# Optimization experiments

Measured on AMD Instinct MI355X. Metric: run time of the kernel, lower is better.

The kernel has to match this reference:

```python
import jax, jax.numpy as jnp
import numpy as np

V = 32000   # vocab / input_size
H = 1024    # hidden_size (== embedding dim)
L = 2       # num_layers
B = 64      # batch
T = 256     # seq_len


def setup_inputs() -> dict:
    key = jax.random.key(0)
    ks = jax.random.split(key, 8)
    s = float(1.0 / np.sqrt(H))  # pytorch default uniform bound for LSTM/Linear
    return {
        "inputs": jax.random.randint(ks[0], (B, T), 0, V),
        "embed_table": jax.random.normal(ks[1], (V, H), jnp.float32),
        "W_ih": jax.random.uniform(ks[2], (L, 4 * H, H), jnp.float32, -s, s),
        "W_hh": jax.random.uniform(ks[3], (L, 4 * H, H), jnp.float32, -s, s),
        "b_ih": jax.random.uniform(ks[4], (L, 4 * H), jnp.float32, -s, s),
        "b_hh": jax.random.uniform(ks[5], (L, 4 * H), jnp.float32, -s, s),
        "W_proj": jax.random.uniform(ks[6], (V, H), jnp.float32, -s, s),
        "b_proj": jnp.zeros((V,), jnp.float32),  # module fills bias with 0
    }


def _lstm_layer(x, Wih, Whh, bih, bhh):
    # x: [B, T, H]. Precompute input contribution for all steps (one big GEMM).
    xg = jnp.einsum("bth,gh->btg", x, Wih) + bih + bhh  # [B, T, 4H]
    h0 = jnp.zeros((x.shape[0], Whh.shape[1]), x.dtype)
    c0 = h0

    def step(carry, xt):
        h, c = carry
        gates = xt + h @ Whh.T  # [B, 4H]
        i, f, g, o = jnp.split(gates, 4, axis=-1)  # pytorch gate order i,f,g,o
        i = jax.nn.sigmoid(i)
        f = jax.nn.sigmoid(f)
        g = jnp.tanh(g)
        o = jax.nn.sigmoid(o)
        c = f * c + i * g
        h = o * jnp.tanh(c)
        return (h, c), h

    (hT, cT), ys = jax.lax.scan(step, (h0, c0), jnp.swapaxes(xg, 0, 1))
    return jnp.swapaxes(ys, 0, 1), hT, cT  # [B,T,H], [B,H], [B,H]


def reference(inputs, embed_table, W_ih, W_hh, b_ih, b_hh, W_proj, b_proj):
    x = embed_table[inputs]  # [B, T, H]
    h_n, c_n = [], []
    for l in range(L):  # small fixed layer loop
        x, hT, cT = _lstm_layer(x, W_ih[l], W_hh[l], b_ih[l], b_hh[l])
        h_n.append(hT)
        c_n.append(cT)
    last_output = x[:, -1]                      # squeeze(output[:, -1]) with B>1 -> [B, H]
    logits = last_output @ W_proj.T + b_proj    # [B, V]
    return last_output, logits, jnp.stack(h_n), jnp.stack(c_n)
```

## Files before the change

kernel.cpp:

```cpp
#include <hip/hip_runtime.h>
#include <hip/hip_bf16.h>
#include <stdint.h>
#include <stddef.h>

typedef __hip_bfloat16 bf16;
typedef __attribute__((ext_vector_type(8))) short bfrag;
typedef __attribute__((ext_vector_type(4))) float ffrag;

#define HDIM 1024
#define BATCH 64
#define TSTEPS 256
#define GDIM 4096
#define VOCAB 32000

#define HSLOT 16384ull

__device__ __forceinline__ float b2f(bf16 x) { return __bfloat162float(x); }
__device__ __forceinline__ bf16 f2b(float x) { return __float2bfloat16(x); }
__device__ __forceinline__ short f2bs(float x) {
  bf16 b = __float2bfloat16(x);
  return *reinterpret_cast<short*>(&b);
}
__device__ __forceinline__ float bs2f(unsigned short u) {
  union { unsigned int i; float f; } v;
  v.i = ((unsigned int)u) << 16;
  return v.f;
}
__device__ __forceinline__ ffrag mfma16(bfrag a, bfrag b, ffrag c) {
  return __builtin_amdgcn_mfma_f32_16x16x32_bf16(a, b, c, 0, 0, 0);
}
__device__ __forceinline__ float sigm(float x) { return 1.0f / (1.0f + __expf(-x)); }
__device__ __forceinline__ float tanhfast(float x) {
  float e = __expf(2.0f * x);
  return 1.0f - 2.0f / (e + 1.0f);
}

__device__ __forceinline__ void store_u16_agent(unsigned short* p, unsigned short v) {
  __hip_atomic_store(p, v, __ATOMIC_RELAXED, __HIP_MEMORY_SCOPE_AGENT);
}
__device__ __forceinline__ unsigned long long load_u64_agent(const unsigned long long* p) {
  return __hip_atomic_load(p, __ATOMIC_RELAXED, __HIP_MEMORY_SCOPE_AGENT);
}
__device__ __forceinline__ void store_u32_agent(unsigned* p, unsigned v) {
  __hip_atomic_store(p, v, __ATOMIC_RELAXED, __HIP_MEMORY_SCOPE_AGENT);
}

__global__ void convert_bf16_kernel(const float* __restrict__ src, bf16* __restrict__ dst, int n4) {
  int i = blockIdx.x * 256 + threadIdx.x;
  if (i >= n4) return;
  float4 v = reinterpret_cast<const float4*>(src)[i];
  ushort4 o;
  o.x = (unsigned short)f2bs(v.x);
  o.y = (unsigned short)f2bs(v.y);
  o.z = (unsigned short)f2bs(v.z);
  o.w = (unsigned short)f2bs(v.w);
  reinterpret_cast<ushort4*>(dst)[i] = o;
}

__global__ void embed_kernel(const int* __restrict__ ids, const float* __restrict__ table,
                             bf16* __restrict__ x, int n4) {
  int i = blockIdx.x * 256 + threadIdx.x;
  if (i >= n4) return;
  int row = i >> 8;
  int c4 = i & 255;
  int tok = ids[row];
  float4 v = reinterpret_cast<const float4*>(table)[(size_t)tok * 256 + c4];
  ushort4 o;
  o.x = (unsigned short)f2bs(v.x);
  o.y = (unsigned short)f2bs(v.y);
  o.z = (unsigned short)f2bs(v.z);
  o.w = (unsigned short)f2bs(v.w);
  reinterpret_cast<ushort4*>(x)[i] = o;
}

#define BMX 128
#define BNX 128
#define BKX 64

template<int LYR>
__launch_bounds__(256, 2)
__global__ void gemm_xg_kernel(const bf16* __restrict__ A,
                               const bf16* __restrict__ W,
                               const float* __restrict__ bih,
                               const float* __restrict__ bhh,
                               bf16* __restrict__ xg) {
  __shared__ bf16 As[BMX][BKX + 8];
  __shared__ bf16 Bs[BNX][BKX + 8];
  const int n0 = blockIdx.x * BNX;
  const int m0 = blockIdx.y * BMX;
  const int tid = threadIdx.x;
  const int w = tid >> 6, l = tid & 63;
  const int wm = (w >> 1) * 64, wn = (w & 1) * 64;
  const int lr = l & 15, lk = (l >> 4) * 8;

  ffrag acc[4][4];
#pragma unroll
  for (int i = 0; i < 4; ++i)
#pragma unroll
    for (int j = 0; j < 4; ++j) acc[i][j] = ffrag{0.f, 0.f, 0.f, 0.f};

  const int sr = tid >> 1, sh = (tid & 1) * 32;
  for (int kb = 0; kb < HDIM; kb += BKX) {
    __syncthreads();
    {
      if (LYR == 0) {
        const uint4* ga = reinterpret_cast<const uint4*>(&A[(size_t)(m0 + sr) * HDIM + kb + sh]);
        uint4* la = reinterpret_cast<uint4*>(&As[sr][sh]);
        la[0] = ga[0]; la[1] = ga[1]; la[2] = ga[2]; la[3] = ga[3];
      } else {
        const unsigned long long* hb = (const unsigned long long*)A;
        const int m = m0 + sr;
        const size_t tb = (size_t)(255 - (m >> 6)) * HSLOT + (m & 63);
        const int kg0 = (kb + sh) >> 3;
#pragma unroll
        for (int ii = 0; ii < 4; ++ii) {
          unsigned long long lo = hb[tb + (size_t)(kg0 + ii) * 64];
          unsigned long long hi = hb[tb + 8192 + (size_t)(kg0 + ii) * 64];
          *(unsigned long long*)&As[sr][sh + ii * 8]     = lo;
          *(unsigned long long*)&As[sr][sh + ii * 8 + 4] = hi;
        }
      }
      const uint4* gb = reinterpret_cast<const uint4*>(&W[(size_t)(n0 + sr) * HDIM + kb + sh]);
      uint4* lb = reinterpret_cast<uint4*>(&Bs[sr][sh]);
      lb[0] = gb[0]; lb[1] = gb[1]; lb[2] = gb[2]; lb[3] = gb[3];
    }
    __syncthreads();
#pragma unroll
    for (int ks = 0; ks < 2; ++ks) {
      const int ko = ks * 32 + lk;
      bfrag af[4], bfv[4];
#pragma unroll
      for (int i = 0; i < 4; ++i)
        af[i] = *reinterpret_cast<const bfrag*>(&As[wm + i * 16 + lr][ko]);
#pragma unroll
      for (int j = 0; j < 4; ++j)
        bfv[j] = *reinterpret_cast<const bfrag*>(&Bs[wn + j * 16 + lr][ko]);
#pragma unroll
      for (int i = 0; i < 4; ++i)
#pragma unroll
        for (int j = 0; j < 4; ++j)
          acc[i][j] = mfma16(af[i], bfv[j], acc[i][j]);
    }
  }
  const int rg = (l >> 4) * 4;
#pragma unroll
  for (int j = 0; j < 4; ++j) {
    const int n = n0 + wn + j * 16 + lr;
    const float bias = bih[n] + bhh[n];
    const int q = n >> 10, g = (n & 1023) >> 3, jj = n & 7;
    bf16* base = xg + (size_t)(q * 128 + g) * 16384 * 8 + jj;
#pragma unroll
    for (int i = 0; i < 4; ++i) {
#pragma unroll
      for (int r = 0; r < 4; ++r) {
        const int m = m0 + wm + i * 16 + rg + r;
        base[(size_t)m * 8] = f2b(acc[i][j][r] + bias);
      }
    }
  }
}

__launch_bounds__(128, 1)
__global__ void lstm_seq_kernel(const bf16* __restrict__ xg,
                                const bf16* __restrict__ Whh,
                                bf16* hist,
                                float* __restrict__ out_h,
                                float* __restrict__ out_c,
                                float* __restrict__ out_last,
                                unsigned* __restrict__ flags,
                                int xbs, int xts) {
  __shared__ float gxp[2][16][33];
  const int wgid = blockIdx.x;
  const int bg = wgid & 3, cg = wgid >> 2;
  const int tid = threadIdx.x;
  const int w = tid >> 6, l = tid & 63;
  const int lr = l & 15, lkg = l >> 4;
  const int kh = w, kbase = kh * 512;

  bfrag breg0[16], breg1[16];
  {
    const int q = lr >> 2, ja = lr & 3;
    const size_t g0 = ((size_t)q * HDIM + cg * 8 + ja) * HDIM + kbase + lkg * 8;
    const size_t g1 = ((size_t)q * HDIM + cg * 8 + 4 + ja) * HDIM + kbase + lkg * 8;
#pragma unroll
    for (int ks = 0; ks < 16; ++ks) {
      breg0[ks] = *reinterpret_cast<const bfrag*>(&Whh[g0 + ks * 32]);
      breg1[ks] = *reinterpret_cast<const bfrag*>(&Whh[g1 + ks * 32]);
    }
  }

  const int eb = tid & 15;
  const int ejj = tid >> 4;
  const int b_glob = bg * 16 + eb;
  const int j_glob = cg * 8 + ejj;
  const int set = ejj >> 2, jn = ejj & 3;
  float c = 0.0f;

  unsigned long long* hb = (unsigned long long*)hist;
  const size_t hbase = (size_t)(kh * 64 + lkg) * 64 + bg * 16 + lr;

  const bf16* xq0 = xg + (size_t)(0 * 128 + cg) * 16384 * 8 + ejj;
  const bf16* xq1 = xg + (size_t)(1 * 128 + cg) * 16384 * 8 + ejj;
  const bf16* xq2 = xg + (size_t)(2 * 128 + cg) * 16384 * 8 + ejj;
  const bf16* xq3 = xg + (size_t)(3 * 128 + cg) * 16384 * 8 + ejj;
  unsigned short xv0, xv1, xv2, xv3;
  {
    const size_t xidx = (size_t)b_glob * xbs;
    xv0 = *(const unsigned short*)&xq0[xidx * 8];
    xv1 = *(const unsigned short*)&xq1[xidx * 8];
    xv2 = *(const unsigned short*)&xq2[xidx * 8];
    xv3 = *(const unsigned short*)&xq3[xidx * 8];
  }

  const unsigned long long* fv = (const unsigned long long*)flags + (size_t)bg * 128;

#pragma unroll 1
  for (int t = 0; t < TSTEPS; ++t) {
    if (t > 0) {
      const unsigned tt = (unsigned)t;
      for (;;) {
        unsigned long long fa = load_u64_agent(&fv[l]);
        unsigned long long fb = load_u64_agent(&fv[64 + l]);
        int ok = ((unsigned)fa >= tt) && ((unsigned)(fa >> 32) >= tt) &&
                 ((unsigned)fb >= tt) && ((unsigned)(fb >> 32) >= tt);
        if (__all(ok)) break;
        __builtin_amdgcn_s_sleep(1);
      }
    }
    __builtin_amdgcn_sched_barrier(0);
    asm volatile("" ::: "memory");

    const unsigned long long* hin = hb + (size_t)(TSTEPS - t) * HSLOT;
    ffrag a0 = ffrag{0.f, 0.f, 0.f, 0.f};
    ffrag a1 = ffrag{0.f, 0.f, 0.f, 0.f};
#pragma unroll
    for (int ks = 0; ks < 16; ++ks) {
      union { unsigned long long u[2]; bfrag f; } au;
      au.u[0] = hin[hbase + ks * 256];
      au.u[1] = hin[8192 + hbase + ks * 256];
      a0 = mfma16(au.f, breg0[ks], a0);
      a1 = mfma16(au.f, breg1[ks], a1);
    }
#pragma unroll
    for (int r = 0; r < 4; ++r) {
      gxp[kh][lkg * 4 + r][lr]      = a0[r];
      gxp[kh][lkg * 4 + r][16 + lr] = a1[r];
    }
    __syncthreads();

    const float gi = gxp[0][eb][set * 16 + jn]      + gxp[1][eb][set * 16 + jn]      + bs2f(xv0);
    const float gf = gxp[0][eb][set * 16 + 4 + jn]  + gxp[1][eb][set * 16 + 4 + jn]  + bs2f(xv1);
    const float gg = gxp[0][eb][set * 16 + 8 + jn]  + gxp[1][eb][set * 16 + 8 + jn]  + bs2f(xv2);
    const float go = gxp[0][eb][set * 16 + 12 + jn] + gxp[1][eb][set * 16 + 12 + jn] + bs2f(xv3);
    const float iv = sigm(gi), fvv = sigm(gf), gv = tanhfast(gg), ov = sigm(go);
    c = fvv * c + iv * gv;
    const float h = ov * tanhfast(c);
    const unsigned short hbits = (unsigned short)f2bs(h);

    unsigned long long* hout = hb + (size_t)(255 - t) * HSLOT;
    unsigned short* hp = (unsigned short*)(hout + (size_t)set * 8192 + cg * 64 + b_glob) + jn;
    store_u16_agent(hp, hbits);

    if (t < TSTEPS - 1) {
      __builtin_amdgcn_s_waitcnt(0);
      if (l == 0) store_u32_agent(&flags[bg * 256 + cg * 2 + w], (unsigned)(t + 1));
      const size_t xidx = (size_t)b_glob * xbs + (size_t)(t + 1) * xts;
      xv0 = *(const unsigned short*)&xq0[xidx * 8];
      xv1 = *(const unsigned short*)&xq1[xidx * 8];
      xv2 = *(const unsigned short*)&xq2[xidx * 8];
      xv3 = *(const unsigned short*)&xq3[xidx * 8];
    } else {
      out_h[(size_t)b_glob * HDIM + j_glob] = h;
      out_c[(size_t)b_glob * HDIM + j_glob] = c;
      if (out_last) out_last[(size_t)b_glob * HDIM + j_glob] = h;
    }
  }
}

__launch_bounds__(256, 2)
__global__ void logits_kernel(const bf16* __restrict__ hfin,
                              const float* __restrict__ Wp,
                              const float* __restrict__ bp,
                              float* __restrict__ out) {
  const int tid = threadIdx.x;
  const int w = tid >> 6, l = tid & 63;
  const int lr = l & 15, lkg = l >> 4, lk = lkg * 8;
  const int col = blockIdx.x * 64 + w * 16 + lr;
  const float* wrow = &Wp[(size_t)col * HDIM];
  const unsigned long long* hb = (const unsigned long long*)hfin;
  ffrag acc[4];
#pragma unroll
  for (int i = 0; i < 4; ++i) acc[i] = ffrag{0.f, 0.f, 0.f, 0.f};
#pragma unroll 2
  for (int ks = 0; ks < 32; ++ks) {
    const int k = ks * 32 + lk;
    float4 wa = *reinterpret_cast<const float4*>(&wrow[k]);
    float4 wb = *reinterpret_cast<const float4*>(&wrow[k + 4]);
    bfrag bv;
    bv[0] = f2bs(wa.x); bv[1] = f2bs(wa.y); bv[2] = f2bs(wa.z); bv[3] = f2bs(wa.w);
    bv[4] = f2bs(wb.x); bv[5] = f2bs(wb.y); bv[6] = f2bs(wb.z); bv[7] = f2bs(wb.w);
    const size_t kg = (size_t)(ks * 4 + lkg);
#pragma unroll
    for (int i = 0; i < 4; ++i) {
      union { unsigned long long u[2]; bfrag f; } av;
      av.u[0] = hb[kg * 64 + i * 16 + lr];
      av.u[1] = hb[8192 + kg * 64 + i * 16 + lr];
      acc[i] = mfma16(av.f, bv, acc[i]);
    }
  }
  const float bias = bp[col];
#pragma unroll
  for (int i = 0; i < 4; ++i) {
#pragma unroll
    for (int r = 0; r < 4; ++r) {
      const int b = i * 16 + (l >> 4) * 4 + r;
      out[(size_t)b * VOCAB + col] = acc[i][r] + bias;
    }
  }
}

extern "C" void kernel_launch(void* const* d_in, const int* in_sizes, int n_in,
                              void* d_out, int out_size, void* d_ws, size_t ws_size,
                              hipStream_t stream) {
  const int*   ids   = (const int*)d_in[0];
  const float* table = (const float*)d_in[1];
  const float* Wih   = (const float*)d_in[2];
  const float* Whh   = (const float*)d_in[3];
  const float* bih   = (const float*)d_in[4];
  const float* bhh   = (const float*)d_in[5];
  const float* Wp    = (const float*)d_in[6];
  const float* bp    = (const float*)d_in[7];
  float* out = (float*)d_out;

  char* ws = (char*)d_ws;
  const size_t HISTB = 257ull * 131072ull;
  const size_t OFF_XG  = 0;
  const size_t OFF_HA  = OFF_XG + (size_t)512 * 16384 * 8 * 2;
  const size_t OFF_HB  = OFF_HA + HISTB;
  const size_t OFF_WIH = OFF_HB + HISTB;
  const size_t OFF_WHH = OFF_WIH + (size_t)2 * GDIM * HDIM * 2;
  const size_t OFF_SYNC= OFF_WHH + (size_t)2 * GDIM * HDIM * 2;

  bf16* xg    = (bf16*)(ws + OFF_XG);
  bf16* xb    = (bf16*)(ws + OFF_HA);
  bf16* histA = (bf16*)(ws + OFF_HA);
  bf16* histB = (bf16*)(ws + OFF_HB);
  bf16* wihb  = (bf16*)(ws + OFF_WIH);
  bf16* whhb  = (bf16*)(ws + OFF_WHH);
  unsigned* sync = (unsigned*)(ws + OFF_SYNC);

  (void)hipMemsetAsync(sync, 0, 16384, stream);
  (void)hipMemsetAsync(ws + OFF_HA + 33554432ull, 0, 131072, stream);
  (void)hipMemsetAsync(ws + OFF_HB + 33554432ull, 0, 131072, stream);

  const int nconv4 = 2 * GDIM * HDIM / 4;
  convert_bf16_kernel<<<nconv4 / 256, 256, 0, stream>>>(Wih, wihb, nconv4);
  convert_bf16_kernel<<<nconv4 / 256, 256, 0, stream>>>(Whh, whhb, nconv4);
  const int nemb4 = BATCH * TSTEPS * HDIM / 4;
  embed_kernel<<<nemb4 / 256, 256, 0, stream>>>(ids, table, xb, nemb4);

  float* out_last   = out;
  float* out_logits = out + 65536;
  float* out_hn     = out + 2113536;
  float* out_cn     = out + 2244608;

  gemm_xg_kernel<0><<<dim3(GDIM / BNX, (BATCH * TSTEPS) / BMX), 256, 0, stream>>>(
      xb, wihb, bih, bhh, xg);
  lstm_seq_kernel<<<512, 128, 0, stream>>>(
      xg, whhb, histA, out_hn, out_cn, nullptr, sync, 256, 1);

  gemm_xg_kernel<1><<<dim3(GDIM / BNX, (BATCH * TSTEPS) / BMX), 256, 0, stream>>>(
      histA, wihb + (size_t)GDIM * HDIM, bih + GDIM, bhh + GDIM, xg);
  lstm_seq_kernel<<<512, 128, 0, stream>>>(
      xg, whhb + (size_t)GDIM * HDIM, histB,
      out_hn + (size_t)BATCH * HDIM, out_cn + (size_t)BATCH * HDIM,
      out_last, sync + 1024, 1, 64);

  logits_kernel<<<VOCAB / 64, 256, 0, stream>>>(histB, Wp, bp, out_logits);
}
```

Measured before the change: 2.315 ms.

## Fuse both LSTM layers into one wavefront-pipelined persistent kernel

Replaces the sequential layer-1 recurrence, layer-2 input GEMM and layer-2 recurrence with a single persistent kernel of 768 blocks in three roles. Layer-1 blocks run the recurrence. Projection blocks compute W_ih2·h1[t] for each step as soon as it is ready and write it to an 8-slot ring buffer. Layer-2 blocks consume that buffer and run their own recurrence. Flag-based agent-scope synchronisation chains the roles so the two layers overlap in time, and each block now handles 32 batch rows instead of 16. The design depends on all 768 blocks being resident at once, and the busy-wait handoffs add latency to each step.

```diff
diff --git a/kernel.cpp b/kernel.cpp
--- a/kernel.cpp
+++ b/kernel.cpp
@@ -15,7 +15,6 @@
 
 #define HSLOT 16384ull
 
-__device__ __forceinline__ float b2f(bf16 x) { return __bfloat162float(x); }
 __device__ __forceinline__ bf16 f2b(float x) { return __float2bfloat16(x); }
 __device__ __forceinline__ short f2bs(float x) {
   bf16 b = __float2bfloat16(x);
@@ -43,6 +42,12 @@
 }
 __device__ __forceinline__ void store_u32_agent(unsigned* p, unsigned v) {
   __hip_atomic_store(p, v, __ATOMIC_RELAXED, __HIP_MEMORY_SCOPE_AGENT);
+}
+__device__ __forceinline__ void store_f32_agent(float* p, float v) {
+  __hip_atomic_store(p, v, __ATOMIC_RELAXED, __HIP_MEMORY_SCOPE_AGENT);
+}
+__device__ __forceinline__ float load_f32_agent(const float* p) {
+  return __hip_atomic_load(p, __ATOMIC_RELAXED, __HIP_MEMORY_SCOPE_AGENT);
 }
 
 __global__ void convert_bf16_kernel(const float* __restrict__ src, bf16* __restrict__ dst, int n4) {
@@ -77,7 +82,6 @@
 #define BNX 128
 #define BKX 64
 
-template<int LYR>
 __launch_bounds__(256, 2)
 __global__ void gemm_xg_kernel(const bf16* __restrict__ A,
                                const bf16* __restrict__ W,
@@ -103,23 +107,9 @@
   for (int kb = 0; kb < HDIM; kb += BKX) {
     __syncthreads();
     {
-      if (LYR == 0) {
-        const uint4* ga = reinterpret_cast<const uint4*>(&A[(size_t)(m0 + sr) * HDIM + kb + sh]);
-        uint4* la = reinterpret_cast<uint4*>(&As[sr][sh]);
-        la[0] = ga[0]; la[1] = ga[1]; la[2] = ga[2]; la[3] = ga[3];
-      } else {
-        const unsigned long long* hb = (const unsigned long long*)A;
-        const int m = m0 + sr;
-        const size_t tb = (size_t)(255 - (m >> 6)) * HSLOT + (m & 63);
-        const int kg0 = (kb + sh) >> 3;
-#pragma unroll
-        for (int ii = 0; ii < 4; ++ii) {
-          unsigned long long lo = hb[tb + (size_t)(kg0 + ii) * 64];
-          unsigned long long hi = hb[tb + 8192 + (size_t)(kg0 + ii) * 64];
-          *(unsigned long long*)&As[sr][sh + ii * 8]     = lo;
-          *(unsigned long long*)&As[sr][sh + ii * 8 + 4] = hi;
-        }
-      }
+      const uint4* ga = reinterpret_cast<const uint4*>(&A[(size_t)(m0 + sr) * HDIM + kb + sh]);
+      uint4* la = reinterpret_cast<uint4*>(&As[sr][sh]);
+      la[0] = ga[0]; la[1] = ga[1]; la[2] = ga[2]; la[3] = ga[3];
       const uint4* gb = reinterpret_cast<const uint4*>(&W[(size_t)(n0 + sr) * HDIM + kb + sh]);
       uint4* lb = reinterpret_cast<uint4*>(&Bs[sr][sh]);
       lb[0] = gb[0]; lb[1] = gb[1]; lb[2] = gb[2]; lb[3] = gb[3];
@@ -160,119 +150,334 @@
   }
 }
 
-__launch_bounds__(128, 1)
-__global__ void lstm_seq_kernel(const bf16* __restrict__ xg,
-                                const bf16* __restrict__ Whh,
-                                bf16* hist,
-                                float* __restrict__ out_h,
-                                float* __restrict__ out_c,
-                                float* __restrict__ out_last,
-                                unsigned* __restrict__ flags,
-                                int xbs, int xts) {
-  __shared__ float gxp[2][16][33];
-  const int wgid = blockIdx.x;
-  const int bg = wgid & 3, cg = wgid >> 2;
+__launch_bounds__(128, 2)
+__global__ void fused_lstm_kernel(const bf16* __restrict__ xg,
+                                  const bf16* __restrict__ whh1,
+                                  const bf16* __restrict__ whh2,
+                                  const bf16* __restrict__ wih2,
+                                  const float* __restrict__ bih2,
+                                  const float* __restrict__ bhh2,
+                                  bf16* histA, bf16* histB,
+                                  float* xpart,
+                                  float* __restrict__ out_h1, float* __restrict__ out_c1,
+                                  float* __restrict__ out_h2, float* __restrict__ out_c2,
+                                  float* __restrict__ out_last,
+                                  unsigned* __restrict__ fL1,
+                                  unsigned* __restrict__ fL2,
+                                  unsigned* __restrict__ fx) {
+  __shared__ float gxp[2][32][33];
+  const int id = blockIdx.x;
   const int tid = threadIdx.x;
   const int w = tid >> 6, l = tid & 63;
   const int lr = l & 15, lkg = l >> 4;
   const int kh = w, kbase = kh * 512;
-
-  bfrag breg0[16], breg1[16];
-  {
-    const int q = lr >> 2, ja = lr & 3;
-    const size_t g0 = ((size_t)q * HDIM + cg * 8 + ja) * HDIM + kbase + lkg * 8;
-    const size_t g1 = ((size_t)q * HDIM + cg * 8 + 4 + ja) * HDIM + kbase + lkg * 8;
-#pragma unroll
-    for (int ks = 0; ks < 16; ++ks) {
-      breg0[ks] = *reinterpret_cast<const bfrag*>(&Whh[g0 + ks * 32]);
-      breg1[ks] = *reinterpret_cast<const bfrag*>(&Whh[g1 + ks * 32]);
-    }
-  }
-
-  const int eb = tid & 15;
-  const int ejj = tid >> 4;
-  const int b_glob = bg * 16 + eb;
-  const int j_glob = cg * 8 + ejj;
-  const int set = ejj >> 2, jn = ejj & 3;
-  float c = 0.0f;
-
-  unsigned long long* hb = (unsigned long long*)hist;
-  const size_t hbase = (size_t)(kh * 64 + lkg) * 64 + bg * 16 + lr;
-
-  const bf16* xq0 = xg + (size_t)(0 * 128 + cg) * 16384 * 8 + ejj;
-  const bf16* xq1 = xg + (size_t)(1 * 128 + cg) * 16384 * 8 + ejj;
-  const bf16* xq2 = xg + (size_t)(2 * 128 + cg) * 16384 * 8 + ejj;
-  const bf16* xq3 = xg + (size_t)(3 * 128 + cg) * 16384 * 8 + ejj;
-  unsigned short xv0, xv1, xv2, xv3;
-  {
-    const size_t xidx = (size_t)b_glob * xbs;
-    xv0 = *(const unsigned short*)&xq0[xidx * 8];
-    xv1 = *(const unsigned short*)&xq1[xidx * 8];
-    xv2 = *(const unsigned short*)&xq2[xidx * 8];
-    xv3 = *(const unsigned short*)&xq3[xidx * 8];
-  }
-
-  const unsigned long long* fv = (const unsigned long long*)flags + (size_t)bg * 128;
+  const int eb = tid & 31, jj2 = tid >> 5;
+
+  if (id < 256) {
+    const int bg = id & 1, cg = id >> 1;
+    const int b_glob = bg * 32 + eb;
+    bfrag breg0[16], breg1[16];
+    {
+      const int q = lr >> 2, ja = lr & 3;
+      const size_t g0 = ((size_t)q * HDIM + cg * 8 + ja) * HDIM + kbase + lkg * 8;
+      const size_t g1 = ((size_t)q * HDIM + cg * 8 + 4 + ja) * HDIM + kbase + lkg * 8;
+#pragma unroll
+      for (int ks = 0; ks < 16; ++ks) {
+        breg0[ks] = *reinterpret_cast<const bfrag*>(&whh1[g0 + ks * 32]);
+        breg1[ks] = *reinterpret_cast<const bfrag*>(&whh1[g1 + ks * 32]);
+      }
+    }
+    float cA = 0.f, cB = 0.f;
+    unsigned long long* hb = (unsigned long long*)histA;
+    const size_t hb0 = (size_t)(kh * 64 + lkg) * 64 + bg * 32 + lr;
+    const size_t hb1 = hb0 + 16;
+    const unsigned long long* fv = (const unsigned long long*)fL1 + (size_t)bg * 128;
+    const unsigned short* xgu = (const unsigned short*)xg;
+    unsigned short xnA[4], xnB[4];
+#pragma unroll
+    for (int qq = 0; qq < 4; ++qq) {
+      const size_t base = (((size_t)qq * 128 + cg) * 16384 + (size_t)b_glob * 256) * 8;
+      xnA[qq] = xgu[base + jj2];
+      xnB[qq] = xgu[base + 4 + jj2];
+    }
 
 #pragma unroll 1
-  for (int t = 0; t < TSTEPS; ++t) {
-    if (t > 0) {
-      const unsigned tt = (unsigned)t;
-      for (;;) {
-        unsigned long long fa = load_u64_agent(&fv[l]);
-        unsigned long long fb = load_u64_agent(&fv[64 + l]);
-        int ok = ((unsigned)fa >= tt) && ((unsigned)(fa >> 32) >= tt) &&
-                 ((unsigned)fb >= tt) && ((unsigned)(fb >> 32) >= tt);
-        if (__all(ok)) break;
-        __builtin_amdgcn_s_sleep(1);
-      }
-    }
-    __builtin_amdgcn_sched_barrier(0);
-    asm volatile("" ::: "memory");
-
-    const unsigned long long* hin = hb + (size_t)(TSTEPS - t) * HSLOT;
-    ffrag a0 = ffrag{0.f, 0.f, 0.f, 0.f};
-    ffrag a1 = ffrag{0.f, 0.f, 0.f, 0.f};
-#pragma unroll
-    for (int ks = 0; ks < 16; ++ks) {
-      union { unsigned long long u[2]; bfrag f; } au;
-      au.u[0] = hin[hbase + ks * 256];
-      au.u[1] = hin[8192 + hbase + ks * 256];
-      a0 = mfma16(au.f, breg0[ks], a0);
-      a1 = mfma16(au.f, breg1[ks], a1);
-    }
-#pragma unroll
-    for (int r = 0; r < 4; ++r) {
-      gxp[kh][lkg * 4 + r][lr]      = a0[r];
-      gxp[kh][lkg * 4 + r][16 + lr] = a1[r];
-    }
-    __syncthreads();
-
-    const float gi = gxp[0][eb][set * 16 + jn]      + gxp[1][eb][set * 16 + jn]      + bs2f(xv0);
-    const float gf = gxp[0][eb][set * 16 + 4 + jn]  + gxp[1][eb][set * 16 + 4 + jn]  + bs2f(xv1);
-    const float gg = gxp[0][eb][set * 16 + 8 + jn]  + gxp[1][eb][set * 16 + 8 + jn]  + bs2f(xv2);
-    const float go = gxp[0][eb][set * 16 + 12 + jn] + gxp[1][eb][set * 16 + 12 + jn] + bs2f(xv3);
-    const float iv = sigm(gi), fvv = sigm(gf), gv = tanhfast(gg), ov = sigm(go);
-    c = fvv * c + iv * gv;
-    const float h = ov * tanhfast(c);
-    const unsigned short hbits = (unsigned short)f2bs(h);
-
-    unsigned long long* hout = hb + (size_t)(255 - t) * HSLOT;
-    unsigned short* hp = (unsigned short*)(hout + (size_t)set * 8192 + cg * 64 + b_glob) + jn;
-    store_u16_agent(hp, hbits);
-
-    if (t < TSTEPS - 1) {
+    for (int t = 0; t < TSTEPS; ++t) {
+      if (t > 0) {
+        const unsigned tt = (unsigned)t;
+        for (;;) {
+          unsigned long long fa = load_u64_agent(&fv[l]);
+          unsigned long long fb = load_u64_agent(&fv[64 + l]);
+          int ok = ((unsigned)fa >= tt) && ((unsigned)(fa >> 32) >= tt) &&
+                   ((unsigned)fb >= tt) && ((unsigned)(fb >> 32) >= tt);
+          if (__all(ok)) break;
+          __builtin_amdgcn_s_sleep(1);
+        }
+      }
+      __builtin_amdgcn_sched_barrier(0);
+      asm volatile("" ::: "memory");
+
+      const unsigned long long* hin = hb + (size_t)(TSTEPS - t) * HSLOT;
+      ffrag a00 = ffrag{0.f,0.f,0.f,0.f}, a01 = ffrag{0.f,0.f,0.f,0.f};
+      ffrag a10 = ffrag{0.f,0.f,0.f,0.f}, a11 = ffrag{0.f,0.f,0.f,0.f};
+#pragma unroll
+      for (int ks = 0; ks < 16; ++ks) {
+        union { unsigned long long u[2]; bfrag f; } r0, r1;
+        r0.u[0] = hin[hb0 + ks * 256];
+        r0.u[1] = hin[8192 + hb0 + ks * 256];
+        r1.u[0] = hin[hb1 + ks * 256];
+        r1.u[1] = hin[8192 + hb1 + ks * 256];
+        a00 = mfma16(r0.f, breg0[ks], a00);
+        a01 = mfma16(r0.f, breg1[ks], a01);
+        a10 = mfma16(r1.f, breg0[ks], a10);
+        a11 = mfma16(r1.f, breg1[ks], a11);
+      }
+#pragma unroll
+      for (int r = 0; r < 4; ++r) {
+        gxp[kh][lkg * 4 + r][lr]           = a00[r];
+        gxp[kh][lkg * 4 + r][16 + lr]      = a01[r];
+        gxp[kh][16 + lkg * 4 + r][lr]      = a10[r];
+        gxp[kh][16 + lkg * 4 + r][16 + lr] = a11[r];
+      }
+      __syncthreads();
+
+      const float giA = gxp[0][eb][jj2]      + gxp[1][eb][jj2]      + bs2f(xnA[0]);
+      const float gfA = gxp[0][eb][4 + jj2]  + gxp[1][eb][4 + jj2]  + bs2f(xnA[1]);
+      const float ggA = gxp[0][eb][8 + jj2]  + gxp[1][eb][8 + jj2]  + bs2f(xnA[2]);
+      const float goA = gxp[0][eb][12 + jj2] + gxp[1][eb][12 + jj2] + bs2f(xnA[3]);
+      const float giB = gxp[0][eb][16 + jj2]      + gxp[1][eb][16 + jj2]      + bs2f(xnB[0]);
+      const float gfB = gxp[0][eb][16 + 4 + jj2]  + gxp[1][eb][16 + 4 + jj2]  + bs2f(xnB[1]);
+      const float ggB = gxp[0][eb][16 + 8 + jj2]  + gxp[1][eb][16 + 8 + jj2]  + bs2f(xnB[2]);
+      const float goB = gxp[0][eb][16 + 12 + jj2] + gxp[1][eb][16 + 12 + jj2] + bs2f(xnB[3]);
+      cA = sigm(gfA) * cA + sigm(giA) * tanhfast(ggA);
+      const float hA = sigm(goA) * tanhfast(cA);
+      cB = sigm(gfB) * cB + sigm(giB) * tanhfast(ggB);
+      const float hB = sigm(goB) * tanhfast(cB);
+
+      unsigned long long* hout = hb + (size_t)(255 - t) * HSLOT;
+      store_u16_agent((unsigned short*)(hout + (size_t)cg * 64 + b_glob) + jj2,
+                      (unsigned short)f2bs(hA));
+      store_u16_agent((unsigned short*)(hout + 8192 + (size_t)cg * 64 + b_glob) + jj2,
+                      (unsigned short)f2bs(hB));
+      if (t == TSTEPS - 1) {
+        const int jA = cg * 8 + jj2;
+        out_h1[(size_t)b_glob * HDIM + jA] = hA;
+        out_h1[(size_t)b_glob * HDIM + jA + 4] = hB;
+        out_c1[(size_t)b_glob * HDIM + jA] = cA;
+        out_c1[(size_t)b_glob * HDIM + jA + 4] = cB;
+      }
       __builtin_amdgcn_s_waitcnt(0);
-      if (l == 0) store_u32_agent(&flags[bg * 256 + cg * 2 + w], (unsigned)(t + 1));
-      const size_t xidx = (size_t)b_glob * xbs + (size_t)(t + 1) * xts;
-      xv0 = *(const unsigned short*)&xq0[xidx * 8];
-      xv1 = *(const unsigned short*)&xq1[xidx * 8];
-      xv2 = *(const unsigned short*)&xq2[xidx * 8];
-      xv3 = *(const unsigned short*)&xq3[xidx * 8];
-    } else {
-      out_h[(size_t)b_glob * HDIM + j_glob] = h;
-      out_c[(size_t)b_glob * HDIM + j_glob] = c;
-      if (out_last) out_last[(size_t)b_glob * HDIM + j_glob] = h;
+      if (l == 0) store_u32_agent(&fL1[bg * 256 + cg * 2 + w], (unsigned)(t + 1));
+      if (t < TSTEPS - 1) {
+#pragma unroll
+        for (int qq = 0; qq < 4; ++qq) {
+          const size_t base =
+              (((size_t)qq * 128 + cg) * 16384 + (size_t)b_glob * 256 + t + 1) * 8;
+          xnA[qq] = xgu[base + jj2];
+          xnB[qq] = xgu[base + 4 + jj2];
+        }
+      }
+      __syncthreads();
+      __builtin_amdgcn_sched_barrier(0);
+    }
+  } else if (id < 512) {
+    const int sid = id - 256;
+    const int bg = sid & 1, cg = sid >> 1;
+    bfrag breg0[16], breg1[16];
+    {
+      const int q = lr >> 2, ja = lr & 3;
+      const size_t g0 = ((size_t)q * HDIM + cg * 8 + ja) * HDIM + kbase + lkg * 8;
+      const size_t g1 = ((size_t)q * HDIM + cg * 8 + 4 + ja) * HDIM + kbase + lkg * 8;
+#pragma unroll
+      for (int ks = 0; ks < 16; ++ks) {
+        breg0[ks] = *reinterpret_cast<const bfrag*>(&wih2[g0 + ks * 32]);
+        breg1[ks] = *reinterpret_cast<const bfrag*>(&wih2[g1 + ks * 32]);
+      }
+    }
+    const unsigned long long* hbA = (const unsigned long long*)histA;
+    const size_t hb0 = (size_t)(kh * 64 + lkg) * 64 + bg * 32 + lr;
+    const size_t hb1 = hb0 + 16;
+    const unsigned long long* fv = (const unsigned long long*)fL1 + (size_t)bg * 128;
+    const unsigned long long* fbp = (const unsigned long long*)fL2 + (size_t)bg * 128 + cg;
+
+#pragma unroll 1
+    for (int t = 0; t < TSTEPS; ++t) {
+      {
+        const unsigned tt = (unsigned)(t + 1);
+        for (;;) {
+          unsigned long long fa = load_u64_agent(&fv[l]);
+          unsigned long long fb = load_u64_agent(&fv[64 + l]);
+          int ok = ((unsigned)fa >= tt) && ((unsigned)(fa >> 32) >= tt) &&
+                   ((unsigned)fb >= tt) && ((unsigned)(fb >> 32) >= tt);
+          if (__all(ok)) break;
+          __builtin_amdgcn_s_sleep(1);
+        }
+      }
+      if (t >= 8) {
+        const unsigned bp = (unsigned)(t - 7);
+        for (;;) {
+          unsigned long long v = load_u64_agent(fbp);
+          if ((unsigned)v >= bp && (unsigned)(v >> 32) >= bp) break;
+          __builtin_amdgcn_s_sleep(1);
+        }
+      }
+      __builtin_amdgcn_sched_barrier(0);
+      asm volatile("" ::: "memory");
+
+      const unsigned long long* yin = hbA + (size_t)(255 - t) * HSLOT;
+      ffrag a00 = ffrag{0.f,0.f,0.f,0.f}, a01 = ffrag{0.f,0.f,0.f,0.f};
+      ffrag a10 = ffrag{0.f,0.f,0.f,0.f}, a11 = ffrag{0.f,0.f,0.f,0.f};
+#pragma unroll
+      for (int ks = 0; ks < 16; ++ks) {
+        union { unsigned long long u[2]; bfrag f; } r0, r1;
+        r0.u[0] = yin[hb0 + ks * 256];
+        r0.u[1] = yin[8192 + hb0 + ks * 256];
+        r1.u[0] = yin[hb1 + ks * 256];
+        r1.u[1] = yin[8192 + hb1 + ks * 256];
+        a00 = mfma16(r0.f, breg0[ks], a00);
+        a01 = mfma16(r0.f, breg1[ks], a01);
+        a10 = mfma16(r1.f, breg0[ks], a10);
+        a11 = mfma16(r1.f, breg1[ks], a11);
+      }
+#pragma unroll
+      for (int r = 0; r < 4; ++r) {
+        gxp[kh][lkg * 4 + r][lr]           = a00[r];
+        gxp[kh][lkg * 4 + r][16 + lr]      = a01[r];
+        gxp[kh][16 + lkg * 4 + r][lr]      = a10[r];
+        gxp[kh][16 + lkg * 4 + r][16 + lr] = a11[r];
+      }
+      __syncthreads();
+#pragma unroll
+      for (int q = 0; q < 4; ++q) {
+        const float vA = gxp[0][eb][q * 4 + jj2]      + gxp[1][eb][q * 4 + jj2];
+        const float vB = gxp[0][eb][16 + q * 4 + jj2] + gxp[1][eb][16 + q * 4 + jj2];
+        const size_t ib =
+            ((((size_t)(t & 7) * 4 + q) * 2 + bg) * 128 + cg) * 256 + (size_t)eb * 8;
+        store_f32_agent(&xpart[ib + jj2], vA);
+        store_f32_agent(&xpart[ib + 4 + jj2], vB);
+      }
+      __builtin_amdgcn_s_waitcnt(0);
+      if (l == 0) store_u32_agent(&fx[bg * 256 + cg * 2 + w], (unsigned)(t + 1));
+      __syncthreads();
+      __builtin_amdgcn_sched_barrier(0);
+    }
+  } else {
+    const int sid = id - 512;
+    const int bg = sid & 1, cg = sid >> 1;
+    const int b_glob = bg * 32 + eb;
+    bfrag breg0[16], breg1[16];
+    {
+      const int q = lr >> 2, ja = lr & 3;
+      const size_t g0 = ((size_t)q * HDIM + cg * 8 + ja) * HDIM + kbase + lkg * 8;
+      const size_t g1 = ((size_t)q * HDIM + cg * 8 + 4 + ja) * HDIM + kbase + lkg * 8;
+#pragma unroll
+      for (int ks = 0; ks < 16; ++ks) {
+        breg0[ks] = *reinterpret_cast<const bfrag*>(&whh2[g0 + ks * 32]);
+        breg1[ks] = *reinterpret_cast<const bfrag*>(&whh2[g1 + ks * 32]);
+      }
+    }
+    float biasA[4], biasB[4];
+#pragma unroll
+    for (int q = 0; q < 4; ++q) {
+      const int jA = q * HDIM + cg * 8 + jj2;
+      biasA[q] = bih2[jA] + bhh2[jA];
+      biasB[q] = bih2[jA + 4] + bhh2[jA + 4];
+    }
+    float cA = 0.f, cB = 0.f;
+    unsigned long long* hb = (unsigned long long*)histB;
+    const size_t hb0 = (size_t)(kh * 64 + lkg) * 64 + bg * 32 + lr;
+    const size_t hb1 = hb0 + 16;
+    const unsigned long long* fv = (const unsigned long long*)fL2 + (size_t)bg * 128;
+    const unsigned long long* fxp = (const unsigned long long*)fx + (size_t)bg * 128 + cg;
+
+#pragma unroll 1
+    for (int t = 0; t < TSTEPS; ++t) {
+      {
+        const unsigned tt = (unsigned)(t + 1);
+        for (;;) {
+          unsigned long long v = load_u64_agent(fxp);
+          if ((unsigned)v >= tt && (unsigned)(v >> 32) >= tt) break;
+          __builtin_amdgcn_s_sleep(1);
+        }
+      }
+      if (t > 0) {
+        const unsigned tt = (unsigned)t;
+        for (;;) {
+          unsigned long long fa = load_u64_agent(&fv[l]);
+          unsigned long long fb = load_u64_agent(&fv[64 + l]);
+          int ok = ((unsigned)fa >= tt) && ((unsigned)(fa >> 32) >= tt) &&
+                   ((unsigned)fb >= tt) && ((unsigned)(fb >> 32) >= tt);
+          if (__all(ok)) break;
+          __builtin_amdgcn_s_sleep(1);
+        }
+      }
+      __builtin_amdgcn_sched_barrier(0);
+      asm volatile("" ::: "memory");
+
+      float xpA[4], xpB[4];
+#pragma unroll
+      for (int q = 0; q < 4; ++q) {
+        const size_t ib =
+            ((((size_t)(t & 7) * 4 + q) * 2 + bg) * 128 + cg) * 256 + (size_t)eb * 8;
+        xpA[q] = load_f32_agent(&xpart[ib + jj2]);
+        xpB[q] = load_f32_agent(&xpart[ib + 4 + jj2]);
+      }
+
+      const unsigned long long* hin = hb + (size_t)(TSTEPS - t) * HSLOT;
+      ffrag a00 = ffrag{0.f,0.f,0.f,0.f}, a01 = ffrag{0.f,0.f,0.f,0.f};
+      ffrag a10 = ffrag{0.f,0.f,0.f,0.f}, a11 = ffrag{0.f,0.f,0.f,0.f};
+#pragma unroll
+      for (int ks = 0; ks < 16; ++ks) {
+        union { unsigned long long u[2]; bfrag f; } r0, r1;
+        r0.u[0] = hin[hb0 + ks * 256];
+        r0.u[1] = hin[8192 + hb0 + ks * 256];
+        r1.u[0] = hin[hb1 + ks * 256];
+        r1.u[1] = hin[8192 + hb1 + ks * 256];
+        a00 = mfma16(r0.f, breg0[ks], a00);
+        a01 = mfma16(r0.f, breg1[ks], a01);
+        a10 = mfma16(r1.f, breg0[ks], a10);
+        a11 = mfma16(r1.f, breg1[ks], a11);
+      }
+#pragma unroll
+      for (int r = 0; r < 4; ++r) {
+        gxp[kh][lkg * 4 + r][lr]           = a00[r];
+        gxp[kh][lkg * 4 + r][16 + lr]      = a01[r];
+        gxp[kh][16 + lkg * 4 + r][lr]      = a10[r];
+        gxp[kh][16 + lkg * 4 + r][16 + lr] = a11[r];
+      }
+      __syncthreads();
+
+      const float giA = gxp[0][eb][jj2]      + gxp[1][eb][jj2]      + xpA[0] + biasA[0];
+      const float gfA = gxp[0][eb][4 + jj2]  + gxp[1][eb][4 + jj2]  + xpA[1] + biasA[1];
+      const float ggA = gxp[0][eb][8 + jj2]  + gxp[1][eb][8 + jj2]  + xpA[2] + biasA[2];
+      const float goA = gxp[0][eb][12 + jj2] + gxp[1][eb][12 + jj2] + xpA[3] + biasA[3];
+      const float giB = gxp[0][eb][16 + jj2]      + gxp[1][eb][16 + jj2]      + xpB[0] + biasB[0];
+      const float gfB = gxp[0][eb][16 + 4 + jj2]  + gxp[1][eb][16 + 4 + jj2]  + xpB[1] + biasB[1];
+      const float ggB = gxp[0][eb][16 + 8 + jj2]  + gxp[1][eb][16 + 8 + jj2]  + xpB[2] + biasB[2];
+      const float goB = gxp[0][eb][16 + 12 + jj2] + gxp[1][eb][16 + 12 + jj2] + xpB[3] + biasB[3];
+      cA = sigm(gfA) * cA + sigm(giA) * tanhfast(ggA);
+      const float hA = sigm(goA) * tanhfast(cA);
+      cB = sigm(gfB) * cB + sigm(giB) * tanhfast(ggB);
+      const float hB = sigm(goB) * tanhfast(cB);
+
+      unsigned long long* hout = hb + (size_t)(255 - t) * HSLOT;
+      store_u16_agent((unsigned short*)(hout + (size_t)cg * 64 + b_glob) + jj2,
+                      (unsigned short)f2bs(hA));
+      store_u16_agent((unsigned short*)(hout + 8192 + (size_t)cg * 64 + b_glob) + jj2,
+                      (unsigned short)f2bs(hB));
+      if (t == TSTEPS - 1) {
+        const int jA = cg * 8 + jj2;
+        out_h2[(size_t)b_glob * HDIM + jA] = hA;
+        out_h2[(size_t)b_glob * HDIM + jA + 4] = hB;
+        out_c2[(size_t)b_glob * HDIM + jA] = cA;
+        out_c2[(size_t)b_glob * HDIM + jA + 4] = cB;
+        out_last[(size_t)b_glob * HDIM + jA] = hA;
+        out_last[(size_t)b_glob * HDIM + jA + 4] = hB;
+      }
+      __builtin_amdgcn_s_waitcnt(0);
+      if (l == 0) store_u32_agent(&fL2[bg * 256 + cg * 2 + w], (unsigned)(t + 1));
+      __syncthreads();
+      __builtin_amdgcn_sched_barrier(0);
     }
   }
 }
@@ -333,11 +538,11 @@
   float* out = (float*)d_out;
 
   char* ws = (char*)d_ws;
-  const size_t HISTB = 257ull * 131072ull;
+  const size_t HISTB_SZ = 257ull * 131072ull;
   const size_t OFF_XG  = 0;
   const size_t OFF_HA  = OFF_XG + (size_t)512 * 16384 * 8 * 2;
-  const size_t OFF_HB  = OFF_HA + HISTB;
-  const size_t OFF_WIH = OFF_HB + HISTB;
+  const size_t OFF_HB  = OFF_HA + HISTB_SZ;
+  const size_t OFF_WIH = OFF_HB + HISTB_SZ;
   const size_t OFF_WHH = OFF_WIH + (size_t)2 * GDIM * HDIM * 2;
   const size_t OFF_SYNC= OFF_WHH + (size_t)2 * GDIM * HDIM * 2;
 
@@ -347,7 +552,11 @@
   bf16* histB = (bf16*)(ws + OFF_HB);
   bf16* wihb  = (bf16*)(ws + OFF_WIH);
   bf16* whhb  = (bf16*)(ws + OFF_WHH);
+  float* xpart = (float*)(ws + OFF_WIH);
   unsigned* sync = (unsigned*)(ws + OFF_SYNC);
+  unsigned* fL1 = sync;
+  unsigned* fL2 = sync + 512;
+  unsigned* fx  = sync + 1024;
 
   (void)hipMemsetAsync(sync, 0, 16384, stream);
   (void)hipMemsetAsync(ws + OFF_HA + 33554432ull, 0, 131072, stream);
@@ -364,17 +573,14 @@
   float* out_hn     = out + 2113536;
   float* out_cn     = out + 2244608;
 
-  gemm_xg_kernel<0><<<dim3(GDIM / BNX, (BATCH * TSTEPS) / BMX), 256, 0, stream>>>(
+  gemm_xg_kernel<<<dim3(GDIM / BNX, (BATCH * TSTEPS) / BMX), 256, 0, stream>>>(
       xb, wihb, bih, bhh, xg);
-  lstm_seq_kernel<<<512, 128, 0, stream>>>(
-      xg, whhb, histA, out_hn, out_cn, nullptr, sync, 256, 1);
-
-  gemm_xg_kernel<1><<<dim3(GDIM / BNX, (BATCH * TSTEPS) / BMX), 256, 0, stream>>>(
-      histA, wihb + (size_t)GDIM * HDIM, bih + GDIM, bhh + GDIM, xg);
-  lstm_seq_kernel<<<512, 128, 0, stream>>>(
-      xg, whhb + (size_t)GDIM * HDIM, histB,
-      out_hn + (size_t)BATCH * HDIM, out_cn + (size_t)BATCH * HDIM,
-      out_last, sync + 1024, 1, 64);
+
+  fused_lstm_kernel<<<768, 128, 0, stream>>>(
+      xg, whhb, whhb + (size_t)GDIM * HDIM, wihb + (size_t)GDIM * HDIM,
+      bih + GDIM, bhh + GDIM, histA, histB, xpart,
+      out_hn, out_cn, out_hn + BATCH * HDIM, out_cn + BATCH * HDIM, out_last,
+      fL1, fL2, fx);
 
   logits_kernel<<<VOCAB / 64, 256, 0, stream>>>(histB, Wp, bp, out_logits);
 }
```

Measured after the change: 2.922 ms. 1.26x slower.
